# Kernel tuning notes

Hardware: AMD Instinct MI355X
Metric: run time of the kernel (lower is better)

The kernel has to match this reference:

```python
import jax, jax.numpy as jnp
import numpy as np

Z_NUM_LIST = [[1,1]]*12 + [[2,1]] + [[2,2]]*11 + [[4,2]] + [[4,4]]*11  # 36 layers
Z_DIM, IN_SZ, OUT_SZ, FS = 64, 16, 16, 3
N_Z = sum(o*i for o, i in Z_NUM_LIST)  # 242
_OFFS = np.concatenate([[0], np.cumsum([o*i for o, i in Z_NUM_LIST])]).astype(int)
BN_EPS = 1e-5


def setup_inputs() -> dict:
    key = jax.random.key(0)
    ks = jax.random.split(key, 8)
    x = jax.random.normal(ks[0], (1024, 3, 32, 32), dtype=jnp.float32)
    conv_w = jax.random.normal(ks[1], (16, 3, 3, 3), dtype=jnp.float32) * 0.1
    conv_b = jnp.zeros((16,), dtype=jnp.float32)
    bn_gamma = jnp.ones((16,), dtype=jnp.float32)
    bn_beta = jnp.zeros((16,), dtype=jnp.float32)
    z_all = jax.random.normal(ks[2], (N_Z, Z_DIM), dtype=jnp.float32)  # 242 z-vectors
    # HyperNet params: z -> (in_sz*z_dim), reshape (in_sz, z_dim), -> (in_sz, out_sz*f*f)
    w2 = jax.random.normal(ks[3], (Z_DIM, IN_SZ * Z_DIM), dtype=jnp.float32) * 0.125
    b2 = jnp.zeros((IN_SZ * Z_DIM,), dtype=jnp.float32)
    w1 = jax.random.normal(ks[4], (Z_DIM, OUT_SZ * FS * FS), dtype=jnp.float32) * 0.125
    b1 = jnp.zeros((OUT_SZ * FS * FS,), dtype=jnp.float32)
    return {"x": x, "conv_w": conv_w, "conv_b": conv_b, "bn_gamma": bn_gamma,
            "bn_beta": bn_beta, "z_all": z_all, "w1": w1, "b1": b1, "w2": w2, "b2": b2}


def _hypernet_batched(z_all, w1, b1, w2, b2):
    # All 242 tiny per-z MLPs as one stacked GEMM pair.
    h_in = (z_all @ w2 + b2).reshape(-1, IN_SZ, Z_DIM)          # [N, 16, 64]
    h_fin = jnp.einsum('nid,do->nio', h_in, w1) + b1            # [N, 16, 144]
    return h_fin.reshape(-1, OUT_SZ, IN_SZ, FS, FS)             # torch .view semantics


def _assemble_weights(kernels):
    # Replicates nested torch.cat(dim=1) then cat(dim=0) per Embedding.
    weights = []
    for li, (o_n, i_n) in enumerate(Z_NUM_LIST):
        k = kernels[_OFFS[li]:_OFFS[li + 1]].reshape(o_n, i_n, OUT_SZ, IN_SZ, FS, FS)
        w = k.transpose(0, 2, 1, 3, 4, 5).reshape(o_n * OUT_SZ, i_n * IN_SZ, FS, FS)
        weights.append(w)
    return weights


def reference(x, conv_w, conv_b, bn_gamma, bn_beta, z_all, w1, b1, w2, b2):
    # conv1 (3->16, 3x3, pad 1)
    y = jax.lax.conv_general_dilated(x, conv_w, (1, 1), 'SAME',
                                     dimension_numbers=('NCHW', 'OIHW', 'NCHW'))
    y = y + conv_b[None, :, None, None]
    # batchnorm (training mode: batch statistics) + relu
    mean = jnp.mean(y, axis=(0, 2, 3))
    var = jnp.var(y, axis=(0, 2, 3))
    y = (y - mean[None, :, None, None]) * jax.lax.rsqrt(var + BN_EPS)[None, :, None, None]
    y = jax.nn.relu(y * bn_gamma[None, :, None, None] + bn_beta[None, :, None, None])
    # hypernetwork weight generation (36 conv weight tensors)
    kernels = _hypernet_batched(z_all, w1, b1, w2, b2)
    weights = _assemble_weights(kernels)
    return (*weights, y)
```

## Files before the change

kernel.cpp:

```cpp
#include <hip/hip_runtime.h>

#define N_Z     242
#define W_ELEMS (N_Z * 2304)
#define NHW_F   1048576.0f

__constant__ int c_offs[37] = {0,1,2,3,4,5,6,7,8,9,10,11,12,14,18,22,26,30,34,38,
                               42,46,50,54,58,66,82,98,114,130,146,162,178,194,210,226,242};
__constant__ int c_isz[36] = {1,1,1,1,1,1,1,1,1,1,1,1, 1, 2,2,2,2,2,2,2,2,2,2,2, 2,
                              4,4,4,4,4,4,4,4,4,4,4};

union Smem1 {
    struct {
        float zsh[64];
        float b1s[144];
        float hin[1024];
        float w1s[64 * 144];
    } h;
    struct {
        float xs[3][34][35];
        float wsm[16][3][3][4];
        float red[4][16][2];
    } c;
};

__global__ __launch_bounds__(256) void fused_hyper_stats(
    const float* __restrict__ x,     const float* __restrict__ cw,
    const float* __restrict__ cb,
    const float* __restrict__ z_all, const float* __restrict__ w1,
    const float* __restrict__ b1,    const float* __restrict__ w2,
    const float* __restrict__ b2,    float* __restrict__ out,
    float* __restrict__ gacc)
{
    __shared__ Smem1 sm;
    const int t = threadIdx.x;

    if (blockIdx.x < N_Z) {
        const int n = blockIdx.x;
        if (t < 64) sm.h.zsh[t] = z_all[n * 64 + t];
        if (t >= 64 && t < 64 + 144) sm.h.b1s[t - 64] = b1[t - 64];
        for (int i = t; i < 64 * 144; i += 256) sm.h.w1s[i] = w1[i];
        __syncthreads();

        float4 a = *(const float4*)(b2 + 4 * t);
        for (int e = 0; e < 64; ++e) {
            const float zv = sm.h.zsh[e];
            const float4 wr = *(const float4*)(w2 + e * 1024 + 4 * t);
            a.x += zv * wr.x; a.y += zv * wr.y; a.z += zv * wr.z; a.w += zv * wr.w;
        }
        *(float4*)(sm.h.hin + 4 * t) = a;
        __syncthreads();

        int li = 0;
        while (n >= c_offs[li + 1]) ++li;
        const int r   = n - c_offs[li];
        const int isz = c_isz[li];
        const int sh  = isz >> 1;
        const int o   = r >> sh;
        const int ii  = r & (isz - 1);
        float* wout = out + (long)c_offs[li] * 2304;

        const int aI = t >> 4, q = t & 15;
        float acc[9];
        #pragma unroll
        for (int j = 0; j < 9; ++j) acc[j] = sm.h.b1s[9 * q + j];
        const float* hp = sm.h.hin + aI * 64;
        const float* wp = sm.h.w1s + 9 * q;
        #pragma unroll 4
        for (int d = 0; d < 64; ++d) {
            const float hv = hp[d];
            #pragma unroll
            for (int j = 0; j < 9; ++j) acc[j] += hv * wp[d * 144 + j];
        }
        float* op = wout + (o * 16 + aI) * (isz * 144) + (ii * 16 + q) * 9;
        #pragma unroll
        for (int j = 0; j < 9; ++j) op[j] = acc[j];
    } else {
        const int n = blockIdx.x - N_Z;
        const float* xp = x + n * 3072;
        for (int idx = t; idx < 3 * 34 * 35; idx += 256) {
            const int ci  = idx / 1190;
            const int rem = idx - ci * 1190;
            const int rr  = rem / 35, cc = rem - rr * 35;
            float v = 0.0f;
            if (rr >= 1 && rr <= 32 && cc >= 1 && cc <= 32)
                v = xp[ci * 1024 + (rr - 1) * 32 + (cc - 1)];
            sm.c.xs[ci][rr][cc] = v;
        }
        for (int idx = t; idx < 432; idx += 256) {
            const int co = idx / 27, r2 = idx - co * 27;
            const int ci = r2 / 9,   r3 = r2 - ci * 9;
            sm.c.wsm[co][ci][r3 / 3][r3 % 3] = cw[idx];
        }
        __syncthreads();

        const int h = t >> 3, w0 = (t & 7) << 2;
        float xv[3][3][6];
        #pragma unroll
        for (int ci = 0; ci < 3; ++ci)
            #pragma unroll
            for (int rr = 0; rr < 3; ++rr)
                #pragma unroll
                for (int j = 0; j < 6; ++j)
                    xv[ci][rr][j] = sm.c.xs[ci][h + rr][w0 + j];

        const int lane = t & 63, wid = t >> 6;
        #pragma unroll
        for (int co = 0; co < 16; ++co) {
            const float bias = cb[co];
            float a0 = bias, a1 = bias, a2 = bias, a3 = bias;
            #pragma unroll
            for (int ci = 0; ci < 3; ++ci)
                #pragma unroll
                for (int rr = 0; rr < 3; ++rr) {
                    const float4 wv = *(const float4*)&sm.c.wsm[co][ci][rr][0];
                    a0 += wv.x * xv[ci][rr][0] + wv.y * xv[ci][rr][1] + wv.z * xv[ci][rr][2];
                    a1 += wv.x * xv[ci][rr][1] + wv.y * xv[ci][rr][2] + wv.z * xv[ci][rr][3];
                    a2 += wv.x * xv[ci][rr][2] + wv.y * xv[ci][rr][3] + wv.z * xv[ci][rr][4];
                    a3 += wv.x * xv[ci][rr][3] + wv.y * xv[ci][rr][4] + wv.z * xv[ci][rr][5];
                }
            float s = a0 + a1 + a2 + a3;
            float qq = a0 * a0 + a1 * a1 + a2 * a2 + a3 * a3;
            #pragma unroll
            for (int off = 32; off > 0; off >>= 1) {
                s  += __shfl_down(s, off);
                qq += __shfl_down(qq, off);
            }
            if (lane == 0) { sm.c.red[wid][co][0] = s; sm.c.red[wid][co][1] = qq; }
        }
        __syncthreads();
        if (t < 32) {
            const int co = t >> 1, which = t & 1;
            const float v = sm.c.red[0][co][which] + sm.c.red[1][co][which] +
                            sm.c.red[2][co][which] + sm.c.red[3][co][which];
            atomicAdd(&gacc[(n & 7) * 32 + which * 16 + co], v);
        }
    }
}

__global__ __launch_bounds__(256) void conv_bn_relu_kernel(
    const float* __restrict__ x,    const float* __restrict__ cw,
    const float* __restrict__ cb,   const float* __restrict__ gacc,
    const float* __restrict__ gamma,const float* __restrict__ beta,
    float* __restrict__ y)
{
    __shared__ float xs[3][34][35];
    __shared__ float wsm[16][3][3][4];
    __shared__ float ssh[32];
    const int n = blockIdx.x, t = threadIdx.x;

    const float* xp = x + n * 3072;
    for (int idx = t; idx < 3 * 34 * 35; idx += 256) {
        const int ci  = idx / 1190;
        const int rem = idx - ci * 1190;
        const int rr  = rem / 35, cc = rem - rr * 35;
        float v = 0.0f;
        if (rr >= 1 && rr <= 32 && cc >= 1 && cc <= 32)
            v = xp[ci * 1024 + (rr - 1) * 32 + (cc - 1)];
        xs[ci][rr][cc] = v;
    }
    for (int idx = t; idx < 432; idx += 256) {
        const int co = idx / 27, r2 = idx - co * 27;
        const int ci = r2 / 9,   r3 = r2 - ci * 9;
        wsm[co][ci][r3 / 3][r3 % 3] = cw[idx];
    }
    if (t < 16) {
        float S = 0.0f, Q = 0.0f;
        #pragma unroll
        for (int k = 0; k < 8; ++k) {
            S += gacc[k * 32 + t];
            Q += gacc[k * 32 + 16 + t];
        }
        const float inv  = 1.0f / NHW_F;
        const float mean = S * inv;
        const float var  = Q * inv - mean * mean;
        const float rs   = rsqrtf(var + 1e-5f);
        const float sc   = gamma[t] * rs;
        ssh[2 * t]     = sc;
        ssh[2 * t + 1] = beta[t] - mean * sc;
    }
    __syncthreads();

    const int h = t >> 3, w0 = (t & 7) << 2;
    float xv[3][3][6];
    #pragma unroll
    for (int ci = 0; ci < 3; ++ci)
        #pragma unroll
        for (int rr = 0; rr < 3; ++rr)
            #pragma unroll
            for (int j = 0; j < 6; ++j)
                xv[ci][rr][j] = xs[ci][h + rr][w0 + j];

    float* yp = y + n * 16384;
    #pragma unroll
    for (int co = 0; co < 16; ++co) {
        const float bias = cb[co];
        float a0 = bias, a1 = bias, a2 = bias, a3 = bias;
        #pragma unroll
        for (int ci = 0; ci < 3; ++ci)
            #pragma unroll
            for (int rr = 0; rr < 3; ++rr) {
                const float4 wv = *(const float4*)&wsm[co][ci][rr][0];
                a0 += wv.x * xv[ci][rr][0] + wv.y * xv[ci][rr][1] + wv.z * xv[ci][rr][2];
                a1 += wv.x * xv[ci][rr][1] + wv.y * xv[ci][rr][2] + wv.z * xv[ci][rr][3];
                a2 += wv.x * xv[ci][rr][2] + wv.y * xv[ci][rr][3] + wv.z * xv[ci][rr][4];
                a3 += wv.x * xv[ci][rr][3] + wv.y * xv[ci][rr][4] + wv.z * xv[ci][rr][5];
            }
        const float sc = ssh[2 * co], sf = ssh[2 * co + 1];
        float4 o4;
        o4.x = fmaxf(0.0f, a0 * sc + sf);
        o4.y = fmaxf(0.0f, a1 * sc + sf);
        o4.z = fmaxf(0.0f, a2 * sc + sf);
        o4.w = fmaxf(0.0f, a3 * sc + sf);
        *(float4*)(yp + co * 1024 + h * 32 + w0) = o4;
    }
}

extern "C" void kernel_launch(void* const* d_in, const int* in_sizes, int n_in,
                              void* d_out, int out_size, void* d_ws, size_t ws_size,
                              hipStream_t stream)
{
    const float* x     = (const float*)d_in[0];
    const float* cw    = (const float*)d_in[1];
    const float* cb    = (const float*)d_in[2];
    const float* gamma = (const float*)d_in[3];
    const float* beta  = (const float*)d_in[4];
    const float* z_all = (const float*)d_in[5];
    const float* w1    = (const float*)d_in[6];
    const float* b1    = (const float*)d_in[7];
    const float* w2    = (const float*)d_in[8];
    const float* b2    = (const float*)d_in[9];

    float* out  = (float*)d_out;
    float* gacc = (float*)d_ws;
    float* y    = out + W_ELEMS;

    fused_hyper_stats<<<N_Z + 1024, 256, 0, stream>>>(x, cw, cb, z_all, w1, b1, w2, b2,
                                                      out, gacc);
    conv_bn_relu_kernel<<<1024, 256, 0, stream>>>(x, cw, cb, gacc, gamma, beta, y);
}
```

Measured before the change: 148.6 us.

## Broadcast conv weights via readlane, DPP wave reductions, drop w1 LDS staging

Conv weights are now read per lane from global memory and broadcast into scalar registers with readlane, replacing the shared-memory weight staging and float4 LDS reads. The wave-level sum reductions switch from shfl_down to DPP row operations. The hypernet blocks stop copying the 36KB w1 matrix into LDS and read it straight from global memory or cache, which shrinks LDS so more blocks can be resident, and launch bounds now request 4 blocks per CU. In exchange the hypernet inner loop depends on cache-served global loads, and tighter register limits may cause spills.

```diff
diff --git a/kernel.cpp b/kernel.cpp
--- a/kernel.cpp
+++ b/kernel.cpp
@@ -9,21 +9,53 @@
 __constant__ int c_isz[36] = {1,1,1,1,1,1,1,1,1,1,1,1, 1, 2,2,2,2,2,2,2,2,2,2,2, 2,
                               4,4,4,4,4,4,4,4,4,4,4};
 
+template<int CTRL, int RMASK>
+__device__ __forceinline__ float dpp_add(float x) {
+    int s = __builtin_amdgcn_update_dpp(0, __float_as_int(x), CTRL, RMASK, 0xF, true);
+    return x + __int_as_float(s);
+}
+__device__ __forceinline__ float wave_sum64(float x) {
+    x = dpp_add<0x111, 0xF>(x);
+    x = dpp_add<0x112, 0xF>(x);
+    x = dpp_add<0x114, 0xF>(x);
+    x = dpp_add<0x118, 0xF>(x);
+    x = dpp_add<0x142, 0xA>(x);
+    x = dpp_add<0x143, 0xC>(x);
+    return x;
+}
+
+__device__ __forceinline__ void stage_x(const float* __restrict__ xp,
+                                        float (*xs)[34][35], int t)
+{
+    for (int idx = t; idx < 3 * 34 * 35; idx += 256) {
+        const int ci  = idx / 1190;
+        const int rem = idx - ci * 1190;
+        const int rr  = rem / 35, cc = rem - rr * 35;
+        float v = 0.0f;
+        if (rr >= 1 && rr <= 32 && cc >= 1 && cc <= 32)
+            v = xp[ci * 1024 + (rr - 1) * 32 + (cc - 1)];
+        xs[ci][rr][cc] = v;
+    }
+}
+
+__device__ __forceinline__ void load_window(const float (*xs)[34][35],
+                                            float xv[3][3][6], int h, int w0)
+{
+    #pragma unroll
+    for (int ci = 0; ci < 3; ++ci)
+        #pragma unroll
+        for (int rr = 0; rr < 3; ++rr)
+            #pragma unroll
+            for (int j = 0; j < 6; ++j)
+                xv[ci][rr][j] = xs[ci][h + rr][w0 + j];
+}
+
 union Smem1 {
-    struct {
-        float zsh[64];
-        float b1s[144];
-        float hin[1024];
-        float w1s[64 * 144];
-    } h;
-    struct {
-        float xs[3][34][35];
-        float wsm[16][3][3][4];
-        float red[4][16][2];
-    } c;
+    struct { float zsh[64]; float hin[1024]; } h;
+    struct { float xs[3][34][35]; float red[4][32]; } c;
 };
 
-__global__ __launch_bounds__(256) void fused_hyper_stats(
+__global__ __launch_bounds__(256, 4) void fused_hyper_stats(
     const float* __restrict__ x,     const float* __restrict__ cw,
     const float* __restrict__ cb,
     const float* __restrict__ z_all, const float* __restrict__ w1,
@@ -37,8 +69,6 @@
     if (blockIdx.x < N_Z) {
         const int n = blockIdx.x;
         if (t < 64) sm.h.zsh[t] = z_all[n * 64 + t];
-        if (t >= 64 && t < 64 + 144) sm.h.b1s[t - 64] = b1[t - 64];
-        for (int i = t; i < 64 * 144; i += 256) sm.h.w1s[i] = w1[i];
         __syncthreads();
 
         float4 a = *(const float4*)(b2 + 4 * t);
@@ -62,9 +92,9 @@
         const int aI = t >> 4, q = t & 15;
         float acc[9];
         #pragma unroll
-        for (int j = 0; j < 9; ++j) acc[j] = sm.h.b1s[9 * q + j];
-        const float* hp = sm.h.hin + aI * 64;
-        const float* wp = sm.h.w1s + 9 * q;
+        for (int j = 0; j < 9; ++j) acc[j] = b1[9 * q + j];
+        const float* __restrict__ hp = sm.h.hin + aI * 64;
+        const float* __restrict__ wp = w1 + 9 * q;
         #pragma unroll 4
         for (int d = 0; d < 64; ++d) {
             const float hv = hp[d];
@@ -76,93 +106,63 @@
         for (int j = 0; j < 9; ++j) op[j] = acc[j];
     } else {
         const int n = blockIdx.x - N_Z;
-        const float* xp = x + n * 3072;
-        for (int idx = t; idx < 3 * 34 * 35; idx += 256) {
-            const int ci  = idx / 1190;
-            const int rem = idx - ci * 1190;
-            const int rr  = rem / 35, cc = rem - rr * 35;
-            float v = 0.0f;
-            if (rr >= 1 && rr <= 32 && cc >= 1 && cc <= 32)
-                v = xp[ci * 1024 + (rr - 1) * 32 + (cc - 1)];
-            sm.c.xs[ci][rr][cc] = v;
-        }
-        for (int idx = t; idx < 432; idx += 256) {
-            const int co = idx / 27, r2 = idx - co * 27;
-            const int ci = r2 / 9,   r3 = r2 - ci * 9;
-            sm.c.wsm[co][ci][r3 / 3][r3 % 3] = cw[idx];
-        }
+        stage_x(x + n * 3072, sm.c.xs, t);
         __syncthreads();
 
         const int h = t >> 3, w0 = (t & 7) << 2;
         float xv[3][3][6];
-        #pragma unroll
-        for (int ci = 0; ci < 3; ++ci)
-            #pragma unroll
-            for (int rr = 0; rr < 3; ++rr)
-                #pragma unroll
-                for (int j = 0; j < 6; ++j)
-                    xv[ci][rr][j] = sm.c.xs[ci][h + rr][w0 + j];
+        load_window(sm.c.xs, xv, h, w0);
 
         const int lane = t & 63, wid = t >> 6;
+        const int wl = (lane < 27) ? lane : (lane < 54 ? lane - 27 : 0);
+
         #pragma unroll
         for (int co = 0; co < 16; ++co) {
+            const float wlv = cw[co * 27 + wl];
+            float w[27];
+            #pragma unroll
+            for (int k = 0; k < 27; ++k)
+                w[k] = __int_as_float(__builtin_amdgcn_readlane(__float_as_int(wlv), k));
+
             const float bias = cb[co];
             float a0 = bias, a1 = bias, a2 = bias, a3 = bias;
             #pragma unroll
             for (int ci = 0; ci < 3; ++ci)
                 #pragma unroll
                 for (int rr = 0; rr < 3; ++rr) {
-                    const float4 wv = *(const float4*)&sm.c.wsm[co][ci][rr][0];
-                    a0 += wv.x * xv[ci][rr][0] + wv.y * xv[ci][rr][1] + wv.z * xv[ci][rr][2];
-                    a1 += wv.x * xv[ci][rr][1] + wv.y * xv[ci][rr][2] + wv.z * xv[ci][rr][3];
-                    a2 += wv.x * xv[ci][rr][2] + wv.y * xv[ci][rr][3] + wv.z * xv[ci][rr][4];
-                    a3 += wv.x * xv[ci][rr][3] + wv.y * xv[ci][rr][4] + wv.z * xv[ci][rr][5];
+                    const int kb = ci * 9 + rr * 3;
+                    a0 += w[kb] * xv[ci][rr][0] + w[kb+1] * xv[ci][rr][1] + w[kb+2] * xv[ci][rr][2];
+                    a1 += w[kb] * xv[ci][rr][1] + w[kb+1] * xv[ci][rr][2] + w[kb+2] * xv[ci][rr][3];
+                    a2 += w[kb] * xv[ci][rr][2] + w[kb+1] * xv[ci][rr][3] + w[kb+2] * xv[ci][rr][4];
+                    a3 += w[kb] * xv[ci][rr][3] + w[kb+1] * xv[ci][rr][4] + w[kb+2] * xv[ci][rr][5];
                 }
-            float s = a0 + a1 + a2 + a3;
-            float qq = a0 * a0 + a1 * a1 + a2 * a2 + a3 * a3;
-            #pragma unroll
-            for (int off = 32; off > 0; off >>= 1) {
-                s  += __shfl_down(s, off);
-                qq += __shfl_down(qq, off);
+            float s = wave_sum64(a0 + a1 + a2 + a3);
+            float qv = wave_sum64(a0 * a0 + a1 * a1 + a2 * a2 + a3 * a3);
+            if (lane == 63) {
+                sm.c.red[wid][co]      = s;
+                sm.c.red[wid][16 + co] = qv;
             }
-            if (lane == 0) { sm.c.red[wid][co][0] = s; sm.c.red[wid][co][1] = qq; }
         }
         __syncthreads();
         if (t < 32) {
-            const int co = t >> 1, which = t & 1;
-            const float v = sm.c.red[0][co][which] + sm.c.red[1][co][which] +
-                            sm.c.red[2][co][which] + sm.c.red[3][co][which];
-            atomicAdd(&gacc[(n & 7) * 32 + which * 16 + co], v);
-        }
-    }
-}
-
-__global__ __launch_bounds__(256) void conv_bn_relu_kernel(
+            const float v = sm.c.red[0][t] + sm.c.red[1][t] +
+                            sm.c.red[2][t] + sm.c.red[3][t];
+            atomicAdd(&gacc[(n & 7) * 32 + t], v);
+        }
+    }
+}
+
+__global__ __launch_bounds__(256, 4) void conv_bn_relu_kernel(
     const float* __restrict__ x,    const float* __restrict__ cw,
     const float* __restrict__ cb,   const float* __restrict__ gacc,
     const float* __restrict__ gamma,const float* __restrict__ beta,
     float* __restrict__ y)
 {
     __shared__ float xs[3][34][35];
-    __shared__ float wsm[16][3][3][4];
     __shared__ float ssh[32];
     const int n = blockIdx.x, t = threadIdx.x;
 
-    const float* xp = x + n * 3072;
-    for (int idx = t; idx < 3 * 34 * 35; idx += 256) {
-        const int ci  = idx / 1190;
-        const int rem = idx - ci * 1190;
-        const int rr  = rem / 35, cc = rem - rr * 35;
-        float v = 0.0f;
-        if (rr >= 1 && rr <= 32 && cc >= 1 && cc <= 32)
-            v = xp[ci * 1024 + (rr - 1) * 32 + (cc - 1)];
-        xs[ci][rr][cc] = v;
-    }
-    for (int idx = t; idx < 432; idx += 256) {
-        const int co = idx / 27, r2 = idx - co * 27;
-        const int ci = r2 / 9,   r3 = r2 - ci * 9;
-        wsm[co][ci][r3 / 3][r3 % 3] = cw[idx];
-    }
+    stage_x(x + n * 3072, xs, t);
     if (t < 16) {
         float S = 0.0f, Q = 0.0f;
         #pragma unroll
@@ -182,28 +182,31 @@
 
     const int h = t >> 3, w0 = (t & 7) << 2;
     float xv[3][3][6];
-    #pragma unroll
-    for (int ci = 0; ci < 3; ++ci)
-        #pragma unroll
-        for (int rr = 0; rr < 3; ++rr)
-            #pragma unroll
-            for (int j = 0; j < 6; ++j)
-                xv[ci][rr][j] = xs[ci][h + rr][w0 + j];
+    load_window(xs, xv, h, w0);
+
+    const int lane = t & 63;
+    const int wl = (lane < 27) ? lane : (lane < 54 ? lane - 27 : 0);
 
     float* yp = y + n * 16384;
     #pragma unroll
     for (int co = 0; co < 16; ++co) {
+        const float wlv = cw[co * 27 + wl];
+        float w[27];
+        #pragma unroll
+        for (int k = 0; k < 27; ++k)
+            w[k] = __int_as_float(__builtin_amdgcn_readlane(__float_as_int(wlv), k));
+
         const float bias = cb[co];
         float a0 = bias, a1 = bias, a2 = bias, a3 = bias;
         #pragma unroll
         for (int ci = 0; ci < 3; ++ci)
             #pragma unroll
             for (int rr = 0; rr < 3; ++rr) {
-                const float4 wv = *(const float4*)&wsm[co][ci][rr][0];
-                a0 += wv.x * xv[ci][rr][0] + wv.y * xv[ci][rr][1] + wv.z * xv[ci][rr][2];
-                a1 += wv.x * xv[ci][rr][1] + wv.y * xv[ci][rr][2] + wv.z * xv[ci][rr][3];
-                a2 += wv.x * xv[ci][rr][2] + wv.y * xv[ci][rr][3] + wv.z * xv[ci][rr][4];
-                a3 += wv.x * xv[ci][rr][3] + wv.y * xv[ci][rr][4] + wv.z * xv[ci][rr][5];
+                const int kb = ci * 9 + rr * 3;
+                a0 += w[kb] * xv[ci][rr][0] + w[kb+1] * xv[ci][rr][1] + w[kb+2] * xv[ci][rr][2];
+                a1 += w[kb] * xv[ci][rr][1] + w[kb+1] * xv[ci][rr][2] + w[kb+2] * xv[ci][rr][3];
+                a2 += w[kb] * xv[ci][rr][2] + w[kb+1] * xv[ci][rr][3] + w[kb+2] * xv[ci][rr][4];
+                a3 += w[kb] * xv[ci][rr][3] + w[kb+1] * xv[ci][rr][4] + w[kb+2] * xv[ci][rr][5];
             }
         const float sc = ssh[2 * co], sf = ssh[2 * co + 1];
         float4 o4;
```

Result: slower. 152.6 us (+2.7%).
